# Kernel optimization log

Measured on AMD Instinct MI355X. Metric: run time of the kernel, lower is better.

## Reference

```python
import jax, jax.numpy as jnp
import numpy as np

HIDDEN = 1024
NEG_INF = jnp.float32(-1e7)


def setup_inputs() -> dict:
    key = jax.random.key(0)
    ks = jax.random.split(key, 9)
    B, S, H = 4, 2048, HIDDEN
    std = 1.0 / np.sqrt(H)
    return {
        "queries": jax.random.normal(ks[0], (B, S, H), jnp.float32),
        "keys": jax.random.normal(ks[1], (B, S, H), jnp.float32),
        "values": jax.random.normal(ks[2], (B, S, H), jnp.float32),
        "Wq": jax.random.uniform(ks[3], (H, H), jnp.float32, -std, std),
        "bq": jax.random.uniform(ks[4], (H,), jnp.float32, -std, std),
        "Wk": jax.random.uniform(ks[5], (H, H), jnp.float32, -std, std),
        "bk": jax.random.uniform(ks[6], (H,), jnp.float32, -std, std),
        "Wv": jax.random.uniform(ks[7], (H, H), jnp.float32, -std, std),
        "bv": jax.random.uniform(ks[8], (H,), jnp.float32, -std, std),
    }


def reference(queries, keys, values, Wq, bq, Wk, bk, Wv, bv):
    # q,k,v: (B, S, H) linear projections (torch Linear: x @ W.T + b)
    q = jnp.einsum('bth,oh->bto', queries, Wq) + bq
    k = jnp.einsum('bsh,oh->bso', keys, Wk) + bk
    v = jnp.einsum('bsh,oh->bso', values, Wv) + bv
    scale = jax.lax.rsqrt(jnp.float32(q.shape[-1] * 0 + Wq.shape[0]))
    # scores[b, s, t] = <k_s, q_t> * scale   (key index s, query index t)
    scores = jnp.einsum('bsh,bth->bst', k, q) * scale
    S, T = scores.shape[1], scores.shape[2]
    # torch.tril(ones * -1e7, diagonal=-1): add -1e7 where s > t (strictly lower)
    mask = jnp.where(jnp.arange(S)[:, None] > jnp.arange(T)[None, :], NEG_INF, 0.0)
    attn = jax.nn.softmax(scores + mask, axis=1)  # softmax over key dim (dim=1)
    context = jnp.einsum('bst,bsh->bth', attn, v)  # (B, T, H)
    return context, attn
```

## Files before the change

### kernel.cpp

```cpp
#include <hip/hip_runtime.h>
#include <math.h>

typedef __bf16 bf16x8 __attribute__((ext_vector_type(8)));
typedef __bf16 bf16x4 __attribute__((ext_vector_type(4)));
typedef float f32x4 __attribute__((ext_vector_type(4)));

#define HD 1024
#define SEQ 2048
#define NB 4
#define WEL (HD * HD)

__device__ inline bf16x8 load8cvt(const __bf16* p) { return *(const bf16x8*)p; }
__device__ inline bf16x8 load8cvt(const float* p) {
    f32x4 a = *(const f32x4*)p;
    f32x4 b = *(const f32x4*)(p + 4);
    bf16x8 r;
#pragma unroll
    for (int i = 0; i < 4; ++i) { r[i] = (__bf16)a[i]; r[i + 4] = (__bf16)b[i]; }
    return r;
}

__device__ inline f32x4 load4f(const float* p) { return *(const f32x4*)p; }
__device__ inline f32x4 load4f(const __bf16* p) {
    bf16x4 v = *(const bf16x4*)p;
    f32x4 r;
#pragma unroll
    for (int i = 0; i < 4; ++i) r[i] = (float)v[i];
    return r;
}

__device__ inline void gld_lds16(const void* g, void* l) {
    __builtin_amdgcn_global_load_lds(
        (const __attribute__((address_space(1))) unsigned int*)g,
        (__attribute__((address_space(3))) unsigned int*)l, 16, 0, 0);
}

template <typename T>
__device__ inline void stage_tile(const T* __restrict__ G, int ld, __bf16* s, int tid)
{
    const int r  = tid >> 3;
    const int co = ((tid & 7) ^ (r & 7)) * 8;
    if constexpr (sizeof(T) == 2) {
        __bf16* dst = s + (tid >> 6) * 512;
#pragma unroll
        for (int c = 0; c < 4; ++c)
            gld_lds16(G + (long)(c * 32 + r) * ld + co, dst + c * 2048);
    } else {
#pragma unroll
        for (int c = 0; c < 4; ++c)
            *(bf16x8*)(s + c * 2048 + tid * 8) = load8cvt(G + (long)(c * 32 + r) * ld + co);
    }
}

__device__ inline bf16x8 frag_read(const __bf16* s, int row, int c)
{
    return *(const bf16x8*)&s[row * 64 + ((c ^ (row & 7)) * 8)];
}

struct Proj3 {
    const void* A[3];
    const void* W[3];
    const float* bias[3];
    __bf16* C[3];
    int vtmask;
};

template <typename TA, typename TW>
__global__ __launch_bounds__(256) void gemm_proj(Proj3 p)
{
    __shared__ __bf16 sA[128 * 64];
    __shared__ __bf16 sB[128 * 64];

    const int tid = threadIdx.x;
    const int L = blockIdx.x;
    const int per = gridDim.x >> 3;
    const int wrk = (L & 7) * per + (L >> 3);
    const int n0 = (wrk & 7) * 128;
    const int m0 = ((wrk >> 3) & 63) * 128;
    const int z  = wrk >> 9;
    const bool vt = (p.vtmask >> z) & 1;

    const TA* Ag = (const TA*)p.A[z] + (long)m0 * HD;
    const TW* Wg = (const TW*)p.W[z] + (long)n0 * HD;
    const float* bias = p.bias[z];
    __bf16* C = p.C[z];

    const int lane = tid & 63;
    const int l15  = lane & 15;
    const int quad = lane >> 4;
    const int wave = tid >> 6;
    const int wm = (wave >> 1) * 64;
    const int wn = (wave & 1) * 64;

    f32x4 acc[4][4];
    const f32x4 zero = {0.f, 0.f, 0.f, 0.f};
#pragma unroll
    for (int i = 0; i < 4; ++i)
#pragma unroll
        for (int j = 0; j < 4; ++j) acc[i][j] = zero;

    for (int kc = 0; kc < HD; kc += 64) {
        stage_tile(Ag + kc, HD, sA, tid);
        stage_tile(Wg + kc, HD, sB, tid);
        __syncthreads();
#pragma unroll
        for (int kk = 0; kk < 64; kk += 32) {
            const int c8 = quad + (kk >> 3);
            bf16x8 af[4], bf[4];
#pragma unroll
            for (int i = 0; i < 4; ++i)
                af[i] = frag_read(sA, wm + i * 16 + l15, c8);
#pragma unroll
            for (int j = 0; j < 4; ++j)
                bf[j] = frag_read(sB, wn + j * 16 + l15, c8);
#pragma unroll
            for (int i = 0; i < 4; ++i)
#pragma unroll
                for (int j = 0; j < 4; ++j)
                    acc[i][j] = __builtin_amdgcn_mfma_f32_16x16x32_bf16(af[i], bf[j], acc[i][j], 0, 0, 0);
        }
        __syncthreads();
    }

#pragma unroll
    for (int j = 0; j < 4; ++j) {
        const int col = n0 + wn + j * 16 + l15;
        const float bv = bias[col];
#pragma unroll
        for (int i = 0; i < 4; ++i) {
#pragma unroll
            for (int r = 0; r < 4; ++r) {
                const int row = m0 + wm + i * 16 + quad * 4 + r;
                const float v = acc[i][j][r] + bv;
                if (vt) {
                    C[(((long)(row >> 11) * HD) + col) * SEQ + (row & (SEQ - 1))] = (__bf16)v;
                } else {
                    C[(long)row * HD + col] = (__bf16)v;
                }
            }
        }
    }
}

template <bool TRI, bool CKLIM, bool EXPSUM, typename OutT>
__global__ __launch_bounds__(256) void gemm_bt(
    const __bf16* __restrict__ A, long strideA, int lda,
    const __bf16* __restrict__ B, long strideB, int ldb,
    OutT* __restrict__ C, long strideC, int ldc,
    float* __restrict__ gsum,
    int K, float alpha)
{
    __shared__ __bf16 sA[128 * 64];
    __shared__ __bf16 sB[128 * 64];
    __shared__ float csum[128];

    const int tid = threadIdx.x;
    const int L = blockIdx.x;
    const int per = gridDim.x >> 3;
    const int wrk = (L & 7) * per + (L >> 3);
    int n0, m0, z;
    if (TRI) {
        const int Lt = wrk % 136;
        z = wrk / 136;
        int tb = (int)((sqrtf(8.f * Lt + 1.f) - 1.f) * 0.5f);
        while ((tb + 1) * (tb + 2) / 2 <= Lt) ++tb;
        while (tb * (tb + 1) / 2 > Lt) --tb;
        const int sb = Lt - tb * (tb + 1) / 2;
        n0 = tb * 128;
        m0 = sb * 128;
    } else {
        n0 = (wrk & 7) * 128;
        m0 = ((wrk >> 3) & 15) * 128;
        z  = wrk >> 7;
    }

    const __bf16* Ag = A + (long)z * strideA + (long)m0 * lda;
    const __bf16* Bg = B + (long)z * strideB + (long)n0 * ldb;
    C += (long)z * strideC;
    if (EXPSUM) {
        gsum += (long)z * SEQ;
        if (tid < 128) csum[tid] = 0.f;
    }

    const int lane = tid & 63;
    const int l15  = lane & 15;
    const int quad = lane >> 4;
    const int wave = tid >> 6;
    const int wm = (wave >> 1) * 64;
    const int wn = (wave & 1) * 64;

    f32x4 acc[4][4];
    const f32x4 zero = {0.f, 0.f, 0.f, 0.f};
#pragma unroll
    for (int i = 0; i < 4; ++i)
#pragma unroll
        for (int j = 0; j < 4; ++j) acc[i][j] = zero;

    const int Kend = CKLIM ? min(K, m0 + 128) : K;

    for (int kc = 0; kc < Kend; kc += 64) {
        stage_tile(Ag + kc, lda, sA, tid);
        stage_tile(Bg + kc, ldb, sB, tid);
        __syncthreads();
#pragma unroll
        for (int kk = 0; kk < 64; kk += 32) {
            const int c8 = quad + (kk >> 3);
            bf16x8 af[4], bf[4];
#pragma unroll
            for (int i = 0; i < 4; ++i)
                af[i] = frag_read(sA, wm + i * 16 + l15, c8);
#pragma unroll
            for (int j = 0; j < 4; ++j)
                bf[j] = frag_read(sB, wn + j * 16 + l15, c8);
#pragma unroll
            for (int i = 0; i < 4; ++i)
#pragma unroll
                for (int j = 0; j < 4; ++j)
                    acc[i][j] = __builtin_amdgcn_mfma_f32_16x16x32_bf16(af[i], bf[j], acc[i][j], 0, 0, 0);
        }
        __syncthreads();
    }

#pragma unroll
    for (int j = 0; j < 4; ++j) {
        const int col = n0 + wn + j * 16 + l15;
        float part = 0.f;
#pragma unroll
        for (int i = 0; i < 4; ++i) {
#pragma unroll
            for (int r = 0; r < 4; ++r) {
                const int row = m0 + wm + i * 16 + quad * 4 + r;
                float v = acc[i][j][r] * alpha;
                if (EXPSUM) {
                    v = __expf(v);
                    if (row <= col) part += v;
                }
                C[(long)row * ldc + col] = (OutT)v;
            }
        }
        if (EXPSUM) atomicAdd(&csum[wn + j * 16 + l15], part);
    }
    if (EXPSUM) {
        __syncthreads();
        if (tid < 128) atomicAdd(&gsum[n0 + tid], csum[tid]);
    }
}

template <typename ET>
__global__ __launch_bounds__(256) void scale_emit(
    const ET* __restrict__ E, float* __restrict__ Out,
    const float* __restrict__ csum, __bf16* __restrict__ AT)
{
    __shared__ __bf16 tile[64][65];
    const int b = blockIdx.z;
    const int t0 = blockIdx.x * 128;
    const int s0 = blockIdx.y * 128;
    const ET* Eb = E + (long)b * SEQ * SEQ;
    float* Ob = Out + (long)b * SEQ * SEQ;
    __bf16* Ab = AT + (long)b * SEQ * SEQ;
    const int tid = threadIdx.x;

    if (s0 > t0 + 127) {
        const f32x4 z4 = {0.f, 0.f, 0.f, 0.f};
        const int c4 = (tid & 31) * 4;
        for (int r = tid >> 5; r < 128; r += 8)
            *(f32x4*)&Ob[(long)(s0 + r) * SEQ + t0 + c4] = z4;
        return;
    }

#pragma unroll
    for (int ds = 0; ds < 2; ++ds) {
#pragma unroll
        for (int dt = 0; dt < 2; ++dt) {
            const int ss = s0 + ds * 64, tt = t0 + dt * 64;
            const int c4 = (tid & 15) * 4;
            const int tcol = tt + c4;
            const f32x4 sv = *(const f32x4*)&csum[(long)b * SEQ + tcol];
            f32x4 inv;
#pragma unroll
            for (int k = 0; k < 4; ++k) inv[k] = 1.0f / sv[k];
#pragma unroll
            for (int r0 = 0; r0 < 64; r0 += 16) {
                const int s = ss + r0 + (tid >> 4);
                f32x4 e = load4f(&Eb[(long)s * SEQ + tcol]);
                f32x4 p;
#pragma unroll
                for (int k = 0; k < 4; ++k)
                    p[k] = (s <= tcol + k) ? e[k] * inv[k] : 0.f;
                *(f32x4*)&Ob[(long)s * SEQ + tcol] = p;
#pragma unroll
                for (int k = 0; k < 4; ++k)
                    tile[r0 + (tid >> 4)][c4 + k] = (__bf16)p[k];
            }
            __syncthreads();
            const int tr = tid >> 2;
            const int sc = (tid & 3) * 16;
            __bf16 v[16];
#pragma unroll
            for (int jj = 0; jj < 16; ++jj) v[jj] = tile[sc + jj][tr];
            *(bf16x8*)&Ab[(long)(tt + tr) * SEQ + ss + sc]     = *(bf16x8*)v;
            *(bf16x8*)&Ab[(long)(tt + tr) * SEQ + ss + sc + 8] = *(bf16x8*)(v + 8);
            __syncthreads();
        }
    }
}

struct CvtJob { const float* in; __bf16* out; int nblk; };
struct Cvt6 { CvtJob j[6]; };
__global__ __launch_bounds__(256) void cvt_bf16(Cvt6 c)
{
    const CvtJob jb = c.j[blockIdx.y];
    if ((int)blockIdx.x >= jb.nblk) return;
    const long i = ((long)blockIdx.x * 256 + threadIdx.x) * 8;
    *(bf16x8*)&jb.out[i] = load8cvt(&jb.in[i]);
}

extern "C" void kernel_launch(void* const* d_in, const int* in_sizes, int n_in,
                              void* d_out, int out_size, void* d_ws, size_t ws_size,
                              hipStream_t stream)
{
    const float* queries = (const float*)d_in[0];
    const float* keys    = (const float*)d_in[1];
    const float* values  = (const float*)d_in[2];
    const float* Wq = (const float*)d_in[3];
    const float* bq = (const float*)d_in[4];
    const float* Wk = (const float*)d_in[5];
    const float* bk = (const float*)d_in[6];
    const float* Wv = (const float*)d_in[7];
    const float* bv = (const float*)d_in[8];

    const long tokens = (long)NB * SEQ;
    const long pe = tokens * HD;
    const size_t SLOT = (size_t)pe * sizeof(__bf16);
    const int ABLK = (int)(pe / 2048);
    const int WBLK = WEL / 2048;

    float* outCtx  = (float*)d_out;
    float* outAttn = outCtx + tokens * HD;
    float* colsum = outCtx;
    __bf16* wb = (__bf16*)outAttn;
    __bf16* Wqb = wb, *Wkb = wb + WEL, *Wvb = wb + 2 * WEL;

    const dim3 blk(256);
    hipMemsetAsync(colsum, 0, (size_t)NB * SEQ * sizeof(float), stream);

    char* w = (char*)d_ws;
    __bf16 *qp, *kp, *vT, *attnT;

    bool ebig = false;
    __bf16* Ebf = nullptr;

    if (ws_size >= 6 * SLOT) {
        __bf16* xq = (__bf16*)w;
        __bf16* xk = (__bf16*)(w + SLOT);
        __bf16* xv = (__bf16*)(w + 2 * SLOT);
        qp = (__bf16*)(w + 3 * SLOT);
        kp = (__bf16*)(w + 4 * SLOT);
        vT = (__bf16*)(w + 5 * SLOT);
        Ebf = (__bf16*)w;
        attnT = (__bf16*)(w + 2 * SLOT);
        ebig = true;

        Cvt6 cv = {{{queries, xq, ABLK}, {keys, xk, ABLK}, {values, xv, ABLK},
                    {Wq, Wqb, WBLK}, {Wk, Wkb, WBLK}, {Wv, Wvb, WBLK}}};
        cvt_bf16<<<dim3(ABLK, 6), blk, 0, stream>>>(cv);
        Proj3 pj = {{xq, xk, xv}, {Wqb, Wkb, Wvb}, {bq, bk, bv}, {qp, kp, vT}, 4};
        gemm_proj<__bf16, __bf16><<<dim3(512 * 3), blk, 0, stream>>>(pj);
    } else if (ws_size >= 4 * SLOT) {
        __bf16* x0 = (__bf16*)w;
        qp = (__bf16*)(w + SLOT);
        kp = (__bf16*)(w + 2 * SLOT);
        __bf16* x1 = (__bf16*)(w + 3 * SLOT);
        vT = x1;
        attnT = (__bf16*)d_ws;

        Cvt6 cv = {{{queries, x0, ABLK}, {keys, x1, ABLK},
                    {Wq, Wqb, WBLK}, {Wk, Wkb, WBLK}, {Wv, Wvb, WBLK},
                    {nullptr, nullptr, 0}}};
        cvt_bf16<<<dim3(ABLK, 5), blk, 0, stream>>>(cv);
        Proj3 pqk = {{x0, x1, nullptr}, {Wqb, Wkb, nullptr}, {bq, bk, nullptr},
                     {qp, kp, nullptr}, 0};
        gemm_proj<__bf16, __bf16><<<dim3(512 * 2), blk, 0, stream>>>(pqk);
        Cvt6 cvv = {{{values, x0, ABLK}, {nullptr, nullptr, 0}, {nullptr, nullptr, 0},
                     {nullptr, nullptr, 0}, {nullptr, nullptr, 0}, {nullptr, nullptr, 0}}};
        cvt_bf16<<<dim3(ABLK, 1), blk, 0, stream>>>(cvv);
        Proj3 pv = {{x0, nullptr, nullptr}, {Wvb, nullptr, nullptr},
                    {bv, nullptr, nullptr}, {vT, nullptr, nullptr}, 1};
        gemm_proj<__bf16, __bf16><<<dim3(512), blk, 0, stream>>>(pv);
    } else {
        qp = (__bf16*)w;
        kp = (__bf16*)(w + SLOT);
        vT = (__bf16*)(w + 2 * SLOT);
        attnT = (__bf16*)d_ws;
        Proj3 pj = {{queries, keys, values}, {Wq, Wk, Wv}, {bq, bk, bv},
                    {qp, kp, vT}, 4};
        gemm_proj<float, float><<<dim3(512 * 3), blk, 0, stream>>>(pj);
    }

    if (ebig) {
        gemm_bt<true, false, true, __bf16><<<dim3(544), blk, 0, stream>>>(
            kp, (long)SEQ * HD, HD, qp, (long)SEQ * HD, HD,
            Ebf, (long)SEQ * SEQ, SEQ, colsum, HD, 0.03125f);
        scale_emit<__bf16><<<dim3(SEQ / 128, SEQ / 128, NB), blk, 0, stream>>>(
            Ebf, outAttn, colsum, attnT);
    } else {
        gemm_bt<true, false, true, float><<<dim3(544), blk, 0, stream>>>(
            kp, (long)SEQ * HD, HD, qp, (long)SEQ * HD, HD,
            outAttn, (long)SEQ * SEQ, SEQ, colsum, HD, 0.03125f);
        scale_emit<float><<<dim3(SEQ / 128, SEQ / 128, NB), blk, 0, stream>>>(
            outAttn, outAttn, colsum, attnT);
    }

    gemm_bt<false, true, false, float><<<dim3(512), blk, 0, stream>>>(
        attnT, (long)SEQ * SEQ, SEQ, vT, (long)HD * SEQ, SEQ,
        outCtx, (long)SEQ * HD, HD, nullptr, SEQ, 1.0f);
}
```

Before: 387.7 us.

## Double-buffer LDS tiles in projection and batched GEMM kernels

Both GEMM kernels now use two LDS buffers for the A and B tiles. The next K-tile is staged while MFMAs run on the current one, which cuts one of the two barriers per iteration. This hides global-load latency behind compute. In exchange LDS use per block doubles to about 64KB, which may lower occupancy. The fp32 path converts through registers synchronously, so it may overlap less than the async gld_lds path.

```diff
diff --git a/kernel.cpp b/kernel.cpp
--- a/kernel.cpp
+++ b/kernel.cpp
@@ -55,6 +55,29 @@
 __device__ inline bf16x8 frag_read(const __bf16* s, int row, int c)
 {
     return *(const bf16x8*)&s[row * 64 + ((c ^ (row & 7)) * 8)];
+}
+
+__device__ inline void mfma_ktile(const __bf16* __restrict__ sa,
+                                  const __bf16* __restrict__ sb,
+                                  int wm, int wn, int l15, int quad,
+                                  f32x4 (&acc)[4][4])
+{
+#pragma unroll
+    for (int kk = 0; kk < 64; kk += 32) {
+        const int c8 = quad + (kk >> 3);
+        bf16x8 af[4], bf[4];
+#pragma unroll
+        for (int i = 0; i < 4; ++i)
+            af[i] = frag_read(sa, wm + i * 16 + l15, c8);
+#pragma unroll
+        for (int j = 0; j < 4; ++j)
+            bf[j] = frag_read(sb, wn + j * 16 + l15, c8);
+#pragma unroll
+        for (int i = 0; i < 4; ++i)
+#pragma unroll
+            for (int j = 0; j < 4; ++j)
+                acc[i][j] = __builtin_amdgcn_mfma_f32_16x16x32_bf16(af[i], bf[j], acc[i][j], 0, 0, 0);
+    }
 }
 
 struct Proj3 {
@@ -68,8 +91,8 @@
 template <typename TA, typename TW>
 __global__ __launch_bounds__(256) void gemm_proj(Proj3 p)
 {
-    __shared__ __bf16 sA[128 * 64];
-    __shared__ __bf16 sB[128 * 64];
+    __shared__ __bf16 sA[2][128 * 64];
+    __shared__ __bf16 sB[2][128 * 64];
 
     const int tid = threadIdx.x;
     const int L = blockIdx.x;
@@ -99,27 +122,20 @@
 #pragma unroll
         for (int j = 0; j < 4; ++j) acc[i][j] = zero;
 
+    stage_tile(Ag, HD, sA[0], tid);
+    stage_tile(Wg, HD, sB[0], tid);
+    __syncthreads();
+
+    int cur = 0;
     for (int kc = 0; kc < HD; kc += 64) {
-        stage_tile(Ag + kc, HD, sA, tid);
-        stage_tile(Wg + kc, HD, sB, tid);
+        const int nxt = kc + 64;
+        if (nxt < HD) {
+            stage_tile(Ag + nxt, HD, sA[cur ^ 1], tid);
+            stage_tile(Wg + nxt, HD, sB[cur ^ 1], tid);
+        }
+        mfma_ktile(sA[cur], sB[cur], wm, wn, l15, quad, acc);
         __syncthreads();
-#pragma unroll
-        for (int kk = 0; kk < 64; kk += 32) {
-            const int c8 = quad + (kk >> 3);
-            bf16x8 af[4], bf[4];
-#pragma unroll
-            for (int i = 0; i < 4; ++i)
-                af[i] = frag_read(sA, wm + i * 16 + l15, c8);
-#pragma unroll
-            for (int j = 0; j < 4; ++j)
-                bf[j] = frag_read(sB, wn + j * 16 + l15, c8);
-#pragma unroll
-            for (int i = 0; i < 4; ++i)
-#pragma unroll
-                for (int j = 0; j < 4; ++j)
-                    acc[i][j] = __builtin_amdgcn_mfma_f32_16x16x32_bf16(af[i], bf[j], acc[i][j], 0, 0, 0);
-        }
-        __syncthreads();
+        cur ^= 1;
     }
 
 #pragma unroll
@@ -150,8 +166,8 @@
     float* __restrict__ gsum,
     int K, float alpha)
 {
-    __shared__ __bf16 sA[128 * 64];
-    __shared__ __bf16 sB[128 * 64];
+    __shared__ __bf16 sA[2][128 * 64];
+    __shared__ __bf16 sB[2][128 * 64];
     __shared__ float csum[128];
 
     const int tid = threadIdx.x;
@@ -198,27 +214,20 @@
 
     const int Kend = CKLIM ? min(K, m0 + 128) : K;
 
+    stage_tile(Ag, lda, sA[0], tid);
+    stage_tile(Bg, ldb, sB[0], tid);
+    __syncthreads();
+
+    int cur = 0;
     for (int kc = 0; kc < Kend; kc += 64) {
-        stage_tile(Ag + kc, lda, sA, tid);
-        stage_tile(Bg + kc, ldb, sB, tid);
+        const int nxt = kc + 64;
+        if (nxt < Kend) {
+            stage_tile(Ag + nxt, lda, sA[cur ^ 1], tid);
+            stage_tile(Bg + nxt, ldb, sB[cur ^ 1], tid);
+        }
+        mfma_ktile(sA[cur], sB[cur], wm, wn, l15, quad, acc);
         __syncthreads();
-#pragma unroll
-        for (int kk = 0; kk < 64; kk += 32) {
-            const int c8 = quad + (kk >> 3);
-            bf16x8 af[4], bf[4];
-#pragma unroll
-            for (int i = 0; i < 4; ++i)
-                af[i] = frag_read(sA, wm + i * 16 + l15, c8);
-#pragma unroll
-            for (int j = 0; j < 4; ++j)
-                bf[j] = frag_read(sB, wn + j * 16 + l15, c8);
-#pragma unroll
-            for (int i = 0; i < 4; ++i)
-#pragma unroll
-                for (int j = 0; j < 4; ++j)
-                    acc[i][j] = __builtin_amdgcn_mfma_f32_16x16x32_bf16(af[i], bf[j], acc[i][j], 0, 0, 0);
-        }
-        __syncthreads();
+        cur ^= 1;
     }
 
 #pragma unroll
```

Measured after the change: 377.0 us. 2.8% less time.
